# Kernel optimization log

Hardware: AMD Instinct MI355X
Metric: run time of the kernel (lower is better)

The kernel has to match this reference:

```python
import jax, jax.numpy as jnp
from jax import lax
import numpy as np

V, D, H, E, L, B = 512, 128, 64, 4, 60, 4096
ADJ = 184  # ((180 + 7) // 8) * 8


def setup_inputs() -> dict:
    key = jax.random.key(0)
    it = iter(jax.random.split(key, 64))

    def nrm(shape, s=0.05):
        return jax.random.normal(next(it), shape, dtype=jnp.float32) * s

    x = jax.random.randint(next(it), (B, L), 0, V, dtype=jnp.int32)
    inp = {"x": x, "emb": nrm((V, D), 0.02).at[0].set(0.0)}  # padding_idx=0 row zero
    for d in ("f", "r"):
        inp[f"w_ih_{d}"] = nrm((4 * H, D)); inp[f"w_hh_{d}"] = nrm((4 * H, H))
        inp[f"b_ih_{d}"] = nrm((4 * H,)); inp[f"b_hh_{d}"] = nrm((4 * H,))
    for p, i_, h_, o_ in (("e", 1, 16, 8), ("l", 1, 16, 8), ("c", V, 32, 16), ("p", 6, 24, 12), ("x", 4, 16, 8)):
        inp[f"{p}_w1"] = nrm((h_, i_)); inp[f"{p}_b1"] = nrm((h_,))
        inp[f"{p}_w2"] = nrm((o_, h_)); inp[f"{p}_b2"] = nrm((o_,))
    inp["fp_w"] = nrm((ADJ, 180)); inp["fp_b"] = nrm((ADJ,))
    inp["attn_w"] = nrm((3 * ADJ, ADJ)); inp["attn_b"] = nrm((3 * ADJ,))
    inp["out_w"] = nrm((ADJ, ADJ)); inp["out_b"] = nrm((ADJ,))
    for i, (o_, i_) in enumerate(((128, ADJ), (64, 128), (32, 64), (E, 32)), 1):
        inp[f"g_w{i}"] = nrm((o_, i_)); inp[f"g_b{i}"] = nrm((o_,))
    return inp


def _mlp2(h, w1, b1, w2, b2):
    return jnp.maximum(h @ w1.T + b1, 0.0) @ w2.T + b2


def _lstm_final(xe, w_ih, w_hh, b_ih, b_hh):
    # torch LSTM gate order i, f, g, o; returns final hidden state [B, H]
    xg = jnp.einsum('bld,gd->blg', xe, w_ih) + b_ih
    h0 = jnp.zeros((xe.shape[0], H), xe.dtype)

    def step(carry, g_t):
        h, c = carry
        g = g_t + h @ w_hh.T + b_hh
        i, f, gg, o = jnp.split(g, 4, axis=-1)
        c = jax.nn.sigmoid(f) * c + jax.nn.sigmoid(i) * jnp.tanh(gg)
        h = jax.nn.sigmoid(o) * jnp.tanh(c)
        return (h, c), None

    (h, _), _ = lax.scan(step, (h0, h0), jnp.swapaxes(xg, 0, 1))
    return h


def _sequence_stats(x):
    # Fully vectorized equivalent of the per-sequence python loops
    f32 = jnp.float32
    mask = x != 0
    vlen = mask.sum(1)                                       # [B]
    vlenf = jnp.maximum(vlen, 1).astype(f32)
    pos = jnp.arange(L)
    # per-row histogram over valid tokens (torch.bincount of valid_seq)
    counts = jnp.zeros((B, V), f32).at[jnp.arange(B)[:, None], x].add(mask.astype(f32))
    probs = counts / jnp.maximum(counts.sum(1, keepdims=True), 1.0)
    entropy = -jnp.sum(probs * jnp.log(probs + 1e-8), axis=1)
    entropy = jnp.where(vlen > 1, entropy, 0.0)
    char_dist = counts / vlenf[:, None]
    # compact valid tokens to the front (torch: seq[seq != 0]), stable argsort
    order = jnp.argsort((~mask).astype(jnp.int32), axis=1)
    cseq = jnp.take_along_axis(x, order, axis=1)
    cseq = jnp.where(pos[None] < vlen[:, None], cseq, 0)
    a, b = cseq[:, :-1], cseq[:, 1:]
    pairmask = pos[: L - 1][None] < (vlen - 1)[:, None]
    den1 = jnp.maximum(vlen - 1, 1).astype(f32)
    repeat = ((a == b) & pairmask).sum(1) / den1
    inc = ((b > a) & pairmask).sum(1) / den1
    dec = ((b < a) & pairmask).sum(1) / den1
    m2 = pos[: L - 2][None] < (vlen - 2)[:, None]
    per = ((cseq[:, :-2] == cseq[:, 2:]) & m2).sum(1) / jnp.maximum(vlen - 2, 1)
    per = jnp.where(vlen >= 4, per, 0.0)
    diversity = (counts > 0).sum(1) / vlenf
    # longest run of equal consecutive tokens via cummax of reset positions
    eq = jnp.concatenate([jnp.zeros((B, 1), bool), (cseq[:, 1:] == cseq[:, :-1]) & (pos[1:][None] < vlen[:, None])], 1)
    lastreset = lax.cummax(jnp.where(eq, -1, pos[None]), axis=1)
    runlen = pos[None] - lastreset + 1
    max_rep = jnp.where(pos[None] < vlen[:, None], runlen, 0).max(1) / vlenf
    pattern = jnp.stack([repeat, inc, dec, per, diversity, max_rep], 1).astype(f32)
    pattern = jnp.where((vlen > 1)[:, None], pattern, 0.0)
    # unique bigrams: sort pair codes, count distinct valid codes
    codes = jnp.where(pairmask, a * V + b, -1)
    s = jnp.sort(codes, axis=1)
    prevc = jnp.concatenate([jnp.full((B, 1), -2, s.dtype), s[:, :-1]], 1)
    comp_ratio = ((s != prevc) & (s >= 0)).sum(1) / den1
    info_density = entropy / jnp.log(jnp.maximum(vlen, 2).astype(f32))
    # local complexity: mean over sliding windows of (#unique / w), w = min(5, len//2)
    wsel = jnp.minimum(5, vlen // 2)
    local = jnp.zeros((B,), f32)
    for w in (2, 3, 4, 5):
        nwin = L - w + 1
        sh = [cseq[:, k:k + nwin] for k in range(w)]
        u = jnp.ones((B, nwin), f32)
        for k in range(1, w):
            isnew = jnp.ones((B, nwin), bool)
            for m in range(k):
                isnew = isnew & (sh[k] != sh[m])
            u = u + isnew
        winmask = pos[:nwin][None] < (vlen - w + 1)[:, None]
        lc = (u * winmask).sum(1) / w / jnp.maximum(vlen - w + 1, 1)
        local = jnp.where(wsel == w, lc, local)
    trans = 1.0 - repeat  # transitions/(len-1) == 1 - repeat_ratio
    complexity = jnp.stack([comp_ratio, info_density, local, trans], 1).astype(f32)
    complexity = jnp.where((vlen > 1)[:, None], complexity, 0.0)
    return entropy, vlen, char_dist, pattern, complexity


def reference(x, emb, w_ih_f, w_hh_f, b_ih_f, b_hh_f, w_ih_r, w_hh_r, b_ih_r, b_hh_r, e_w1, e_b1, e_w2, e_b2, l_w1, l_b1, l_w2, l_b2, c_w1, c_b1, c_w2, c_b2, p_w1, p_b1, p_w2, p_b2, x_w1, x_b1, x_w2, x_b2, fp_w, fp_b, attn_w, attn_b, out_w, out_b, g_w1, g_b1, g_w2, g_b2, g_w3, g_b3, g_w4, g_b4):
    entropy, vlen, char_dist, pattern, complexity = _sequence_stats(x)
    xe = emb[x]                                               # [B, L, D]
    h_f = _lstm_final(xe, w_ih_f, w_hh_f, b_ih_f, b_hh_f)
    h_r = _lstm_final(xe[:, ::-1], w_ih_r, w_hh_r, b_ih_r, b_hh_r)
    feats = jnp.concatenate([
        h_f, h_r,
        _mlp2((entropy / 4.0)[:, None], e_w1, e_b1, e_w2, e_b2),
        _mlp2((vlen.astype(jnp.float32) / 60.0)[:, None], l_w1, l_b1, l_w2, l_b2),
        _mlp2(char_dist, c_w1, c_b1, c_w2, c_b2),
        _mlp2(pattern, p_w1, p_b1, p_w2, p_b2),
        _mlp2(complexity, x_w1, x_b1, x_w2, x_b2),
    ], axis=1)                                                # [B, 180]
    f = feats @ fp_w.T + fp_b                                 # [B, 184]
    # MultiheadAttention with seq_len == 1: softmax over a single key is 1,
    # so attended = out_proj(v_proj(f)) exactly (q/k projections cancel).
    wv, bv = attn_w[2 * ADJ:], attn_b[2 * ADJ:]
    attended = (f @ wv.T + bv) @ out_w.T + out_b
    h = jnp.maximum(attended @ g_w1.T + g_b1, 0.0)
    h = jnp.maximum(h @ g_w2.T + g_b2, 0.0)
    h = jnp.maximum(h @ g_w3.T + g_b3, 0.0)
    logits = h @ g_w4.T + g_b4
    return jax.nn.softmax(logits, axis=-1)  # eval path (training=False)
```

## Files before the change

### kernel.cpp

```cpp
#include <hip/hip_runtime.h>

#define BATCH 4096
#define SEQL  60
#define VOC   512
#define EMBD  128
#define HID   64
#define GATES 256
#define ADJ   184

typedef __attribute__((ext_vector_type(8))) short short8;
typedef __attribute__((ext_vector_type(4))) float f32x4;

__device__ __forceinline__ float sigm(float x) {
  return __builtin_amdgcn_rcpf(1.f + __expf(-x));
}
__device__ __forceinline__ float tanh_(float x) {
  float e = __expf(2.f * x);
  return 1.f - 2.f * __builtin_amdgcn_rcpf(e + 1.f);
}
__device__ __forceinline__ unsigned short f2bf_rne(float f) {
  unsigned int u = __float_as_uint(f);
  unsigned int r = (u + 0x7fffu + ((u >> 16) & 1u)) >> 16;
  return (unsigned short)r;
}
__device__ __forceinline__ unsigned short f2bf(float f) {
  return (unsigned short)((__float_as_uint(f) + 0x8000u) >> 16);
}
__device__ __forceinline__ float dot4(float4 a, float4 b, float acc) {
  acc = fmaf(a.x, b.x, acc); acc = fmaf(a.y, b.y, acc);
  acc = fmaf(a.z, b.z, acc); acc = fmaf(a.w, b.w, acc);
  return acc;
}
__device__ __forceinline__ float wsumf(float v) {
  #pragma unroll
  for (int s = 32; s > 0; s >>= 1) v += __shfl_xor(v, s, 64);
  return v;
}
__device__ __forceinline__ int wsumi(int v) {
  #pragma unroll
  for (int s = 32; s > 0; s >>= 1) v += __shfl_xor(v, s, 64);
  return v;
}
__device__ __forceinline__ int wmaxi(int v) {
  #pragma unroll
  for (int s = 32; s > 0; s >>= 1) v = max(v, __shfl_xor(v, s, 64));
  return v;
}

__global__ __launch_bounds__(256) void k_prep(
    const float* __restrict__ emb,
    const float* __restrict__ wih_f, const float* __restrict__ bif, const float* __restrict__ bhf,
    const float* __restrict__ wih_r, const float* __restrict__ bir, const float* __restrict__ bhr,
    const float* __restrict__ whh_f, const float* __restrict__ whh_r,
    const float* __restrict__ g_w1, const float* __restrict__ g_b1,
    const float* __restrict__ out_w, const float* __restrict__ out_b,
    const float* __restrict__ attn_w, const float* __restrict__ attn_b,
    const float* __restrict__ fp_w, const float* __restrict__ fp_b,
    const float* __restrict__ g_w2, const float* __restrict__ g_w3,
    const float* __restrict__ g_w4, const float* __restrict__ c_w1,
    float* __restrict__ G_f, float* __restrict__ G_r,
    unsigned short* __restrict__ Wfrag,
    float* __restrict__ A, float* __restrict__ avb,
    float* __restrict__ Bp, float* __restrict__ vb,
    float* __restrict__ g_w2t, float* __restrict__ g_w3t, float* __restrict__ g_w4t,
    float* __restrict__ c_w1t) {
  const int bid = blockIdx.x;
  const int tid = threadIdx.x;

  if (bid < 128) {
    const int dir = bid >> 6;
    const int rem = bid & 63;
    const int v0 = (rem >> 2) * 32;
    const int j0 = (rem & 3) * 64;
    const float* W = dir ? wih_r : wih_f;
    const float* bi = dir ? bir : bif;
    const float* bh = dir ? bhr : bhf;
    float* G = dir ? G_r : G_f;
    const int vp = tid >> 4;
    const int jq = tid & 15;
    const int v = v0 + vp * 2;
    const int j = j0 + jq * 4;
    const int gg = j >> 6;
    const int u0 = j & 63;

    const float4* E0 = (const float4*)(emb + (size_t)v * 128);
    const float4* E1 = (const float4*)(emb + (size_t)(v + 1) * 128);
    const float4* W0 = (const float4*)(W + (size_t)j * 128);
    const float4* W1 = (const float4*)(W + (size_t)(j + 1) * 128);
    const float4* W2 = (const float4*)(W + (size_t)(j + 2) * 128);
    const float4* W3 = (const float4*)(W + (size_t)(j + 3) * 128);

    float a00 = 0.f, a01 = 0.f, a02 = 0.f, a03 = 0.f;
    float a10 = 0.f, a11 = 0.f, a12 = 0.f, a13 = 0.f;
    #pragma unroll 4
    for (int d4 = 0; d4 < 32; d4++) {
      float4 e0 = E0[d4], e1 = E1[d4];
      float4 w0 = W0[d4], w1 = W1[d4], w2 = W2[d4], w3 = W3[d4];
      a00 = dot4(e0, w0, a00); a01 = dot4(e0, w1, a01);
      a02 = dot4(e0, w2, a02); a03 = dot4(e0, w3, a03);
      a10 = dot4(e1, w0, a10); a11 = dot4(e1, w1, a11);
      a12 = dot4(e1, w2, a12); a13 = dot4(e1, w3, a13);
    }
    float b0v = bi[j] + bh[j], b1v = bi[j + 1] + bh[j + 1];
    float b2v = bi[j + 2] + bh[j + 2], b3v = bi[j + 3] + bh[j + 3];
    float* g0 = G + (size_t)v * 256 + u0 * 4 + gg;
    g0[0]  = a00 + b0v; g0[4]  = a01 + b1v;
    g0[8]  = a02 + b2v; g0[12] = a03 + b3v;
    float* g1 = g0 + 256;
    g1[0]  = a10 + b0v; g1[4]  = a11 + b1v;
    g1[8]  = a12 + b2v; g1[12] = a13 + b3v;
  } else if (bid < 144) {
    const int id = (bid - 128) * 256 + tid;
    const int lane = id & 63;
    const int fc = id >> 6;
    const int c = fc & 1;
    const int gg = (fc >> 1) & 3;
    const int w = (fc >> 3) & 3;
    const int dir = fc >> 5;
    const float* whh = dir ? whh_r : whh_f;
    const int n = gg * 64 + w * 16 + (lane & 15);
    const int kb = c * 32 + (lane >> 4) * 8;
    unsigned short* o = Wfrag + (size_t)id * 8;
    #pragma unroll
    for (int j = 0; j < 8; j++) o[j] = f2bf_rne(whh[n * 64 + kb + j]);
  } else if (bid < 272) {
    const int i = bid - 144;
    const int j = tid;
    const float* g1r = g_w1 + (size_t)i * ADJ;
    if (j < ADJ) {
      float a0 = 0.f, a1 = 0.f, a2 = 0.f, a3 = 0.f;
      for (int k = 0; k < ADJ; k += 4) {
        a0 = fmaf(g1r[k],     out_w[(size_t)(k)     * ADJ + j], a0);
        a1 = fmaf(g1r[k + 1], out_w[(size_t)(k + 1) * ADJ + j], a1);
        a2 = fmaf(g1r[k + 2], out_w[(size_t)(k + 2) * ADJ + j], a2);
        a3 = fmaf(g1r[k + 3], out_w[(size_t)(k + 3) * ADJ + j], a3);
      }
      A[(size_t)i * ADJ + j] = (a0 + a1) + (a2 + a3);
    } else if (j == ADJ) {
      float a0 = 0.f;
      for (int k = 0; k < ADJ; k++) a0 = fmaf(g1r[k], out_b[k], a0);
      avb[i] = a0 + g_b1[i];
    }
  } else if (bid < 456) {
    const int k = bid - 272;
    const int j = tid;
    const float* wvr = attn_w + (size_t)(2 * ADJ + k) * ADJ;
    if (j < 180) {
      float a0 = 0.f, a1 = 0.f, a2 = 0.f, a3 = 0.f;
      for (int m = 0; m < ADJ; m += 4) {
        a0 = fmaf(wvr[m],     fp_w[(size_t)(m)     * 180 + j], a0);
        a1 = fmaf(wvr[m + 1], fp_w[(size_t)(m + 1) * 180 + j], a1);
        a2 = fmaf(wvr[m + 2], fp_w[(size_t)(m + 2) * 180 + j], a2);
        a3 = fmaf(wvr[m + 3], fp_w[(size_t)(m + 3) * 180 + j], a3);
      }
      Bp[(size_t)k * 180 + j] = (a0 + a1) + (a2 + a3);
    } else if (j == 180) {
      float a0 = 0.f;
      for (int m = 0; m < ADJ; m++) a0 = fmaf(wvr[m], fp_b[m], a0);
      vb[k] = a0 + attn_b[2 * ADJ + k];
    }
  } else if (bid == 456) {
    for (int i = tid; i < 64 * 128; i += 256) {
      int o = i >> 7, k = i & 127;
      g_w2t[k * 64 + o] = g_w2[i];
    }
    for (int i = tid; i < 32 * 64; i += 256) {
      int o = i >> 6, k = i & 63;
      g_w3t[k * 32 + o] = g_w3[i];
    }
    if (tid < 128) {
      int o = tid >> 5, k = tid & 31;
      g_w4t[k * 4 + o] = g_w4[tid];
    }
  } else {
    const int base = (bid - 457) * 2048;
    for (int i = tid; i < 2048; i += 256) {
      int idx = base + i;
      int o = idx >> 9, k = idx & 511;
      c_w1t[k * 32 + o] = k ? c_w1[o * 512 + k] : 0.f;
    }
  }
}

#define LSTM_STEP(T, CUR, NXT)                                                 \
  {                                                                            \
    const unsigned short* hb = hbuf[(T) & 1];                                  \
    short8 a0 = *(const short8*)(hb + ln * 72 + kg * 8);                       \
    short8 a1 = *(const short8*)(hb + ln * 72 + 32 + kg * 8);                  \
    if ((T) < 59) {                                                            \
      int tsn = dir ? (58 - (T)) : ((T) + 1);                                  \
      uint4 of4 = *(const uint4*)(tokoff + tsn * 16 + kg * 4);                 \
      NXT[0] = *(const float4*)(Gb + of4.x + ub);                              \
      NXT[1] = *(const float4*)(Gb + of4.y + ub);                              \
      NXT[2] = *(const float4*)(Gb + of4.z + ub);                              \
      NXT[3] = *(const float4*)(Gb + of4.w + ub);                              \
    }                                                                          \
    f32x4 z0 = {0.f, 0.f, 0.f, 0.f};                                           \
    f32x4 acc0 = z0, acc1 = z0, acc2 = z0, acc3 = z0;                          \
    acc0 = __builtin_amdgcn_mfma_f32_16x16x32_bf16(a0, bfr[0][0], acc0, 0, 0, 0); \
    acc1 = __builtin_amdgcn_mfma_f32_16x16x32_bf16(a0, bfr[1][0], acc1, 0, 0, 0); \
    acc2 = __builtin_amdgcn_mfma_f32_16x16x32_bf16(a0, bfr[2][0], acc2, 0, 0, 0); \
    acc3 = __builtin_amdgcn_mfma_f32_16x16x32_bf16(a0, bfr[3][0], acc3, 0, 0, 0); \
    acc0 = __builtin_amdgcn_mfma_f32_16x16x32_bf16(a1, bfr[0][1], acc0, 0, 0, 0); \
    acc1 = __builtin_amdgcn_mfma_f32_16x16x32_bf16(a1, bfr[1][1], acc1, 0, 0, 0); \
    acc2 = __builtin_amdgcn_mfma_f32_16x16x32_bf16(a1, bfr[2][1], acc2, 0, 0, 0); \
    acc3 = __builtin_amdgcn_mfma_f32_16x16x32_bf16(a1, bfr[3][1], acc3, 0, 0, 0); \
    unsigned short* hw = hbuf[((T) + 1) & 1];                                  \
    _Pragma("unroll")                                                          \
    for (int r = 0; r < 4; r++) {                                              \
      float gi = acc0[r] + CUR[r].x;                                           \
      float gf = acc1[r] + CUR[r].y;                                           \
      float gc = acc2[r] + CUR[r].z;                                           \
      float go = acc3[r] + CUR[r].w;                                           \
      float cn = sigm(gf) * cst[r] + sigm(gi) * tanh_(gc);                     \
      cst[r] = cn;                                                             \
      float h = sigm(go) * tanh_(cn);                                          \
      hw[(kg * 4 + r) * 72 + u] = f2bf(h);                                     \
      if ((T) == 59) ho[(size_t)(b0 + kg * 4 + r) * 64 + u] = h;               \
    }                                                                          \
    __syncthreads();                                                           \
  }

__global__ __launch_bounds__(256) void k_main(
    const int* __restrict__ x,
    const float* __restrict__ G_f, const float* __restrict__ G_r,
    const unsigned short* __restrict__ Wfrag,
    const float* __restrict__ A, const float* __restrict__ avb,
    const float* __restrict__ Bp, const float* __restrict__ vb,
    float* __restrict__ C1t, float* __restrict__ c1b,
    float* __restrict__ hf_o, float* __restrict__ hr_o,
    float* __restrict__ ent_o, float* __restrict__ vlen_o,
    float* __restrict__ pat_o, float* __restrict__ cpx_o) {
  __shared__ __align__(16) unsigned short hbuf[2][16 * 72];
  __shared__ __align__(16) unsigned int tokoff[60 * 16];
  __shared__ unsigned int cnt[4][512];
  __shared__ unsigned short q[4][68];
  const int bid = blockIdx.x;
  const int tid = threadIdx.x;

  if (bid < 512) {
    const int lane = tid & 63;
    const int w = tid >> 6;
    const int dir = bid >> 8;
    const int blk = bid & 255;
    const int b0 = blk << 4;
    const float* G = dir ? G_r : G_f;
    const char* Gb = (const char*)G;
    float* ho = dir ? hr_o : hf_o;

    for (int i = tid; i < 960; i += 256) {
      int r = i / 60, t = i - r * 60;
      tokoff[t * 16 + r] = ((unsigned int)x[(size_t)(b0 + r) * 60 + t]) << 10;
    }
    for (int i = tid; i < 16 * 72; i += 256) hbuf[0][i] = 0;

    short8 bfr[4][2];
    #pragma unroll
    for (int gg = 0; gg < 4; gg++)
      #pragma unroll
      for (int c = 0; c < 2; c++) {
        int idx = (((dir * 4 + w) * 4 + gg) * 2 + c) * 64 + lane;
        bfr[gg][c] = *(const short8*)(Wfrag + (size_t)idx * 8);
      }

    const int kg = lane >> 4;
    const int ln = lane & 15;
    const int u = w * 16 + ln;
    const unsigned int ub = (unsigned int)u * 16;
    float cst[4] = {0.f, 0.f, 0.f, 0.f};
    float4 gvA[4], gvB[4];

    __syncthreads();

    {
      int ts0 = dir ? 59 : 0;
      uint4 of4 = *(const uint4*)(tokoff + ts0 * 16 + kg * 4);
      gvA[0] = *(const float4*)(Gb + of4.x + ub);
      gvA[1] = *(const float4*)(Gb + of4.y + ub);
      gvA[2] = *(const float4*)(Gb + of4.z + ub);
      gvA[3] = *(const float4*)(Gb + of4.w + ub);
    }

    #pragma unroll 1
    for (int tt = 0; tt < 30; tt++) {
      const int t0 = tt * 2, t1 = tt * 2 + 1;
      LSTM_STEP(t0, gvA, gvB)
      LSTM_STEP(t1, gvB, gvA)
    }
  } else if (bid < 1536) {
    const int lane = tid & 63;
    const int wid = tid >> 6;
    const int row = (bid - 512) * 4 + wid;
    unsigned int* cr = cnt[wid];
    unsigned short* qr = q[wid];

    for (int i = lane; i < 512; i += 64) cr[i] = 0u;
    qr[lane] = 0;
    if (lane < 4) qr[64 + lane] = 0;
    int v = (lane < 60) ? x[row * 60 + lane] : 0;
    bool act = (v != 0);
    unsigned long long amask = __ballot(act);
    int n = __popcll(amask);
    __syncthreads();
    if (act) {
      int pos = __popcll(amask & ((1ull << lane) - 1ull));
      qr[pos] = (unsigned short)v;
      atomicAdd(&cr[v], 1u);
    }
    __syncthreads();

    float vlenf = (float)(n >= 1 ? n : 1);
    float inv = 1.f / vlenf;

    float ent = 0.f; int distinct = 0;
    #pragma unroll
    for (int j = 0; j < 8; j++) {
      unsigned int c = cr[lane + j * 64];
      if (c) {
        distinct++;
        float p = (float)c * inv;
        ent -= p * __logf(p + 1e-8f);
      }
    }
    ent = wsumf(ent);
    distinct = wsumi(distinct);

    int a = qr[lane], b = qr[lane + 1], c2 = qr[lane + 2];
    bool v1 = (lane + 1 < n);
    bool v2 = (lane + 2 < n);
    int rep  = __popcll(__ballot(v1 && (a == b)));
    int incs = __popcll(__ballot(v1 && (b > a)));
    int decs = __popcll(__ballot(v1 && (b < a)));
    int per2 = __popcll(__ballot(v2 && (a == c2)));

    int prev = (lane > 0) ? (int)qr[lane - 1] : -1;
    bool isst = (lane < n) && (lane == 0 || a != prev);
    unsigned long long smask = __ballot(isst);
    int len = 0;
    if (isst) {
      unsigned long long hi = (lane < 63) ? (smask >> (lane + 1)) : 0ull;
      int next = hi ? (lane + __ffsll((unsigned long long)hi)) : n;
      len = next - lane;
    }
    int maxrun = wmaxi(len);

    int code = v1 ? (a * VOC + b) : -1;
    int unique = v1 ? 1 : 0;
    #pragma unroll 1
    for (int j = 0; j < 58; j++) {
      int cj = __shfl(code, j, 64);
      if (j < lane && cj == code) unique = 0;
    }
    int dc = __popcll(__ballot(unique != 0));

    int wl = n >> 1; if (wl > 5) wl = 5;
    float local = 0.f;
    if (wl >= 2) {
      bool pv = (lane + wl <= n);
      int u = 0;
      if (pv) {
        int t0 = qr[lane], t1 = qr[lane + 1], t2 = qr[lane + 2];
        int t3 = qr[lane + 3], t4 = qr[lane + 4];
        u = 1;
        u += (t1 != t0);
        if (wl >= 3) u += (int)((t2 != t1) && (t2 != t0));
        if (wl >= 4) u += (int)((t3 != t2) && (t3 != t1) && (t3 != t0));
        if (wl >= 5) u += (int)((t4 != t3) && (t4 != t2) && (t4 != t1) && (t4 != t0));
      }
      int usum = wsumi(u);
      int denw = n - wl + 1; if (denw < 1) denw = 1;
      local = (float)usum / (float)wl / (float)denw;
    }

    float den1 = (float)((n - 1) >= 1 ? (n - 1) : 1);
    float repeat = (float)rep / den1;
    float per = (n >= 4) ? (float)per2 / (float)((n - 2) >= 1 ? (n - 2) : 1) : 0.f;
    float entz = (n > 1) ? ent : 0.f;
    float z = (n > 1) ? 1.f : 0.f;

    if (lane == 0) {
      ent_o[row] = entz;
      vlen_o[row] = (float)n;
      pat_o[row * 6 + 0] = repeat * z;
      pat_o[row * 6 + 1] = (float)incs / den1 * z;
      pat_o[row * 6 + 2] = (float)decs / den1 * z;
      pat_o[row * 6 + 3] = per * z;
      pat_o[row * 6 + 4] = (float)distinct * inv * z;
      pat_o[row * 6 + 5] = (float)maxrun * inv * z;
      cpx_o[row * 4 + 0] = (float)dc / den1 * z;
      cpx_o[row * 4 + 1] = entz / __logf((float)(n >= 2 ? n : 2)) * z;
      cpx_o[row * 4 + 2] = local * z;
      cpx_o[row * 4 + 3] = (1.f - repeat) * z;
    }
  } else {
    const int i = bid - 1536, j = tid;
    const float* Ar = A + (size_t)i * ADJ;
    if (j < 180) {
      float a0 = 0.f, a1 = 0.f, a2 = 0.f, a3 = 0.f;
      for (int k = 0; k < ADJ; k += 4) {
        a0 = fmaf(Ar[k],     Bp[(size_t)(k)     * 180 + j], a0);
        a1 = fmaf(Ar[k + 1], Bp[(size_t)(k + 1) * 180 + j], a1);
        a2 = fmaf(Ar[k + 2], Bp[(size_t)(k + 2) * 180 + j], a2);
        a3 = fmaf(Ar[k + 3], Bp[(size_t)(k + 3) * 180 + j], a3);
      }
      C1t[(size_t)j * 128 + i] = (a0 + a1) + (a2 + a3);
    } else if (j == 180) {
      float a0 = 0.f;
      for (int k = 0; k < ADJ; k++) a0 = fmaf(Ar[k], vb[k], a0);
      c1b[i] = a0 + avb[i];
    }
  }
}

#define FSTR 192

__global__ __launch_bounds__(256) void k_head(
    const int* __restrict__ x,
    const float* __restrict__ hf, const float* __restrict__ hr,
    const float* __restrict__ ent, const float* __restrict__ vlen,
    const float* __restrict__ pat, const float* __restrict__ cpx,
    const float* __restrict__ e_w1, const float* __restrict__ e_b1,
    const float* __restrict__ e_w2, const float* __restrict__ e_b2,
    const float* __restrict__ l_w1, const float* __restrict__ l_b1,
    const float* __restrict__ l_w2, const float* __restrict__ l_b2,
    const float* __restrict__ c_w1t, const float* __restrict__ c_b1,
    const float* __restrict__ c_w2, const float* __restrict__ c_b2,
    const float* __restrict__ p_w1, const float* __restrict__ p_b1,
    const float* __restrict__ p_w2, const float* __restrict__ p_b2,
    const float* __restrict__ x_w1, const float* __restrict__ x_b1,
    const float* __restrict__ x_w2, const float* __restrict__ x_b2,
    const float* __restrict__ C1t, const float* __restrict__ c1b,
    const float* __restrict__ g_w2t, const float* __restrict__ g_b2,
    const float* __restrict__ g_w3t, const float* __restrict__ g_b3,
    const float* __restrict__ g_w4t, const float* __restrict__ g_b4,
    float* __restrict__ out) {
  __shared__ float feat[8 * FSTR];
  __shared__ unsigned short tk[8 * 64];
  __shared__ float h1[8 * 128];
  __shared__ float h2[8 * 64];
  __shared__ float h3[8 * 32];
  __shared__ float h1c[8 * 33];
  __shared__ float lg[32];
  const int tid = threadIdx.x;
  const int b0 = blockIdx.x * 8;

  if (tid < 128) {
    int r = tid >> 4, c = tid & 15;
    float4 vv = ((const float4*)(hf + (size_t)(b0 + r) * 64))[c];
    *(float4*)(feat + r * FSTR + c * 4) = vv;
  } else {
    int t = tid - 128;
    int r = t >> 4, c = t & 15;
    float4 vv = ((const float4*)(hr + (size_t)(b0 + r) * 64))[c];
    *(float4*)(feat + r * FSTR + 64 + c * 4) = vv;
  }
  for (int i = tid; i < 480; i += 256) {
    int r = i / 60, t = i - r * 60;
    tk[r * 64 + t] = (unsigned short)x[(size_t)(b0 + r) * 60 + t];
  }
  __syncthreads();
  {
    int o = tid & 31, r = tid >> 5;
    const unsigned short* tkr = tk + r * 64;
    float a0 = 0.f, a1 = 0.f, a2 = 0.f, a3 = 0.f;
    #pragma unroll 5
    for (int t = 0; t < 60; t += 4) {
      int t0 = tkr[t], t1 = tkr[t + 1], t2 = tkr[t + 2], t3 = tkr[t + 3];
      a0 += c_w1t[t0 * 32 + o];
      a1 += c_w1t[t1 * 32 + o];
      a2 += c_w1t[t2 * 32 + o];
      a3 += c_w1t[t3 * 32 + o];
    }
    float invv = __builtin_amdgcn_rcpf(fmaxf(vlen[b0 + r], 1.f));
    h1c[r * 33 + o] = fmaxf(((a0 + a1) + (a2 + a3)) * invv + c_b1[o], 0.f);
  }
  __syncthreads();
  if (tid < 32) {
    const int m = tid & 3, r = tid >> 2, b = b0 + r;
    float tt[24];
    if (m == 0) {
      float ein = ent[b] * 0.25f;
      #pragma unroll
      for (int o = 0; o < 16; o++) tt[o] = fmaxf(e_w1[o] * ein + e_b1[o], 0.f);
      #pragma unroll
      for (int o = 0; o < 8; o++) {
        float a = e_b2[o];
        #pragma unroll
        for (int k = 0; k < 16; k++) a = fmaf(e_w2[o * 16 + k], tt[k], a);
        feat[r * FSTR + 128 + o] = a;
      }
    } else if (m == 1) {
      float lin = vlen[b] * (1.f / 60.f);
      #pragma unroll
      for (int o = 0; o < 16; o++) tt[o] = fmaxf(l_w1[o] * lin + l_b1[o], 0.f);
      #pragma unroll
      for (int o = 0; o < 8; o++) {
        float a = l_b2[o];
        #pragma unroll
        for (int k = 0; k < 16; k++) a = fmaf(l_w2[o * 16 + k], tt[k], a);
        feat[r * FSTR + 136 + o] = a;
      }
    } else if (m == 2) {
      float pin[6];
      #pragma unroll
      for (int k = 0; k < 6; k++) pin[k] = pat[b * 6 + k];
      #pragma unroll
      for (int o = 0; o < 24; o++) {
        float a = p_b1[o];
        #pragma unroll
        for (int k = 0; k < 6; k++) a = fmaf(p_w1[o * 6 + k], pin[k], a);
        tt[o] = fmaxf(a, 0.f);
      }
      #pragma unroll
      for (int o = 0; o < 12; o++) {
        float a = p_b2[o];
        #pragma unroll
        for (int k = 0; k < 24; k++) a = fmaf(p_w2[o * 24 + k], tt[k], a);
        feat[r * FSTR + 160 + o] = a;
      }
    } else {
      float xin[4];
      #pragma unroll
      for (int k = 0; k < 4; k++) xin[k] = cpx[b * 4 + k];
      #pragma unroll
      for (int o = 0; o < 16; o++) {
        float a = x_b1[o];
        #pragma unroll
        for (int k = 0; k < 4; k++) a = fmaf(x_w1[o * 4 + k], xin[k], a);
        tt[o] = fmaxf(a, 0.f);
      }
      #pragma unroll
      for (int o = 0; o < 8; o++) {
        float a = x_b2[o];
        #pragma unroll
        for (int k = 0; k < 16; k++) a = fmaf(x_w2[o * 16 + k], tt[k], a);
        feat[r * FSTR + 172 + o] = a;
      }
    }
  } else if (tid >= 64 && tid < 192) {
    int t = tid - 64;
    int r = t >> 4, o = t & 15;
    float a = c_b2[o];
    const float* hh = h1c + r * 33;
    #pragma unroll
    for (int k = 0; k < 32; k++) a = fmaf(c_w2[o * 32 + k], hh[k], a);
    feat[r * FSTR + 144 + o] = a;
  }
  __syncthreads();

  {
    const int o = tid & 127, rg = tid >> 7;
    const float* f0p = feat + (rg * 4 + 0) * FSTR;
    const float* f1p = feat + (rg * 4 + 1) * FSTR;
    const float* f2p = feat + (rg * 4 + 2) * FSTR;
    const float* f3p = feat + (rg * 4 + 3) * FSTR;
    float a0 = 0.f, a1 = 0.f, a2 = 0.f, a3 = 0.f;
    #pragma unroll 3
    for (int k4 = 0; k4 < 45; k4++) {
      float w0 = C1t[(size_t)(k4 * 4 + 0) * 128 + o];
      float w1 = C1t[(size_t)(k4 * 4 + 1) * 128 + o];
      float w2 = C1t[(size_t)(k4 * 4 + 2) * 128 + o];
      float w3 = C1t[(size_t)(k4 * 4 + 3) * 128 + o];
      float4 f0 = *(const float4*)(f0p + k4 * 4);
      float4 f1 = *(const float4*)(f1p + k4 * 4);
      float4 f2 = *(const float4*)(f2p + k4 * 4);
      float4 f3 = *(const float4*)(f3p + k4 * 4);
      a0 = fmaf(w0, f0.x, a0); a0 = fmaf(w1, f0.y, a0);
      a0 = fmaf(w2, f0.z, a0); a0 = fmaf(w3, f0.w, a0);
      a1 = fmaf(w0, f1.x, a1); a1 = fmaf(w1, f1.y, a1);
      a1 = fmaf(w2, f1.z, a1); a1 = fmaf(w3, f1.w, a1);
      a2 = fmaf(w0, f2.x, a2); a2 = fmaf(w1, f2.y, a2);
      a2 = fmaf(w2, f2.z, a2); a2 = fmaf(w3, f2.w, a2);
      a3 = fmaf(w0, f3.x, a3); a3 = fmaf(w1, f3.y, a3);
      a3 = fmaf(w2, f3.z, a3); a3 = fmaf(w3, f3.w, a3);
    }
    float bb = c1b[o];
    h1[(rg * 4 + 0) * 128 + o] = fmaxf(a0 + bb, 0.f);
    h1[(rg * 4 + 1) * 128 + o] = fmaxf(a1 + bb, 0.f);
    h1[(rg * 4 + 2) * 128 + o] = fmaxf(a2 + bb, 0.f);
    h1[(rg * 4 + 3) * 128 + o] = fmaxf(a3 + bb, 0.f);
  }
  __syncthreads();
  {
    const int o = tid & 63, rg = tid >> 6;
    const float* f0p = h1 + (rg * 2 + 0) * 128;
    const float* f1p = h1 + (rg * 2 + 1) * 128;
    float a0 = 0.f, a1 = 0.f;
    #pragma unroll 4
    for (int k4 = 0; k4 < 32; k4++) {
      float w0 = g_w2t[(k4 * 4 + 0) * 64 + o];
      float w1 = g_w2t[(k4 * 4 + 1) * 64 + o];
      float w2 = g_w2t[(k4 * 4 + 2) * 64 + o];
      float w3 = g_w2t[(k4 * 4 + 3) * 64 + o];
      float4 f0 = *(const float4*)(f0p + k4 * 4);
      float4 f1 = *(const float4*)(f1p + k4 * 4);
      a0 = fmaf(w0, f0.x, a0); a0 = fmaf(w1, f0.y, a0);
      a0 = fmaf(w2, f0.z, a0); a0 = fmaf(w3, f0.w, a0);
      a1 = fmaf(w0, f1.x, a1); a1 = fmaf(w1, f1.y, a1);
      a1 = fmaf(w2, f1.z, a1); a1 = fmaf(w3, f1.w, a1);
    }
    float bb = g_b2[o];
    h2[(rg * 2 + 0) * 64 + o] = fmaxf(a0 + bb, 0.f);
    h2[(rg * 2 + 1) * 64 + o] = fmaxf(a1 + bb, 0.f);
  }
  __syncthreads();
  {
    const int o = tid & 31, rg = tid >> 5;
    const float* fp = h2 + rg * 64;
    float a = 0.f;
    #pragma unroll 4
    for (int k4 = 0; k4 < 16; k4++) {
      float w0 = g_w3t[(k4 * 4 + 0) * 32 + o];
      float w1 = g_w3t[(k4 * 4 + 1) * 32 + o];
      float w2 = g_w3t[(k4 * 4 + 2) * 32 + o];
      float w3 = g_w3t[(k4 * 4 + 3) * 32 + o];
      float4 f0 = *(const float4*)(fp + k4 * 4);
      a = fmaf(w0, f0.x, a); a = fmaf(w1, f0.y, a);
      a = fmaf(w2, f0.z, a); a = fmaf(w3, f0.w, a);
    }
    h3[rg * 32 + o] = fmaxf(a + g_b3[o], 0.f);
  }
  __syncthreads();
  if (tid < 32) {
    int r = tid >> 2, o = tid & 3;
    const float* hh = h3 + r * 32;
    float a = g_b4[o];
    #pragma unroll
    for (int k = 0; k < 32; k++) a = fmaf(g_w4t[k * 4 + o], hh[k], a);
    lg[tid] = a;
  }
  __syncthreads();
  if (tid < 8) {
    float l0 = lg[tid * 4 + 0], l1 = lg[tid * 4 + 1];
    float l2 = lg[tid * 4 + 2], l3 = lg[tid * 4 + 3];
    float m = fmaxf(fmaxf(l0, l1), fmaxf(l2, l3));
    float e0 = __expf(l0 - m), e1 = __expf(l1 - m);
    float e2 = __expf(l2 - m), e3 = __expf(l3 - m);
    float is = __builtin_amdgcn_rcpf(e0 + e1 + e2 + e3);
    float4 o4; o4.x = e0 * is; o4.y = e1 * is; o4.z = e2 * is; o4.w = e3 * is;
    *(float4*)(out + (size_t)(b0 + tid) * 4) = o4;
  }
}

extern "C" void kernel_launch(void* const* d_in, const int* in_sizes, int n_in,
                              void* d_out, int out_size, void* d_ws, size_t ws_size,
                              hipStream_t stream) {
  const int*   x     = (const int*)d_in[0];
  const float* emb   = (const float*)d_in[1];
  const float* wih_f = (const float*)d_in[2];
  const float* whh_f = (const float*)d_in[3];
  const float* bih_f = (const float*)d_in[4];
  const float* bhh_f = (const float*)d_in[5];
  const float* wih_r = (const float*)d_in[6];
  const float* whh_r = (const float*)d_in[7];
  const float* bih_r = (const float*)d_in[8];
  const float* bhh_r = (const float*)d_in[9];
  const float* e_w1 = (const float*)d_in[10]; const float* e_b1 = (const float*)d_in[11];
  const float* e_w2 = (const float*)d_in[12]; const float* e_b2 = (const float*)d_in[13];
  const float* l_w1 = (const float*)d_in[14]; const float* l_b1 = (const float*)d_in[15];
  const float* l_w2 = (const float*)d_in[16]; const float* l_b2 = (const float*)d_in[17];
  const float* c_w1 = (const float*)d_in[18]; const float* c_b1 = (const float*)d_in[19];
  const float* c_w2 = (const float*)d_in[20]; const float* c_b2 = (const float*)d_in[21];
  const float* p_w1 = (const float*)d_in[22]; const float* p_b1 = (const float*)d_in[23];
  const float* p_w2 = (const float*)d_in[24]; const float* p_b2 = (const float*)d_in[25];
  const float* x_w1 = (const float*)d_in[26]; const float* x_b1 = (const float*)d_in[27];
  const float* x_w2 = (const float*)d_in[28]; const float* x_b2 = (const float*)d_in[29];
  const float* fp_w = (const float*)d_in[30]; const float* fp_b = (const float*)d_in[31];
  const float* attn_w = (const float*)d_in[32]; const float* attn_b = (const float*)d_in[33];
  const float* out_w = (const float*)d_in[34]; const float* out_b = (const float*)d_in[35];
  const float* g_w1 = (const float*)d_in[36]; const float* g_b1 = (const float*)d_in[37];
  const float* g_w2 = (const float*)d_in[38]; const float* g_b2 = (const float*)d_in[39];
  const float* g_w3 = (const float*)d_in[40]; const float* g_b3 = (const float*)d_in[41];
  const float* g_w4 = (const float*)d_in[42]; const float* g_b4 = (const float*)d_in[43];

  float* ws   = (float*)d_ws;
  float* G_f  = ws;
  float* G_r  = G_f  + 512 * 256;
  float* hfw  = G_r  + 512 * 256;
  float* hrw  = hfw  + BATCH * 64;
  float* entw = hrw  + BATCH * 64;
  float* vlnw = entw + BATCH;
  float* patw = vlnw + BATCH;
  float* cpxw = patw + BATCH * 6;
  float* Aw   = cpxw + BATCH * 4;
  float* avbw = Aw + 128 * ADJ;
  float* Bpw  = avbw + 128;
  float* vbw  = Bpw + ADJ * 180;
  float* C1t  = vbw + ADJ;
  float* c1b  = C1t + 180 * 128;
  float* g2t  = c1b + 128;
  float* g3t  = g2t + 128 * 64;
  float* g4t  = g3t + 64 * 32;
  float* cw1t = g4t + 32 * 4;
  unsigned short* Wfrag = (unsigned short*)(cw1t + 512 * 32);

  k_prep<<<dim3(465), dim3(256), 0, stream>>>(
      emb, wih_f, bih_f, bhh_f, wih_r, bih_r, bhh_r, whh_f, whh_r,
      g_w1, g_b1, out_w, out_b, attn_w, attn_b, fp_w, fp_b,
      g_w2, g_w3, g_w4, c_w1,
      G_f, G_r, Wfrag, Aw, avbw, Bpw, vbw, g2t, g3t, g4t, cw1t);
  k_main<<<dim3(1664), dim3(256), 0, stream>>>(
      x, G_f, G_r, Wfrag, Aw, avbw, Bpw, vbw, C1t, c1b,
      hfw, hrw, entw, vlnw, patw, cpxw);
  k_head<<<dim3(BATCH / 8), dim3(256), 0, stream>>>(
      x, hfw, hrw, entw, vlnw, patw, cpxw,
      e_w1, e_b1, e_w2, e_b2, l_w1, l_b1, l_w2, l_b2,
      cw1t, c_b1, c_w2, c_b2, p_w1, p_b1, p_w2, p_b2,
      x_w1, x_b1, x_w2, x_b2, C1t, c1b,
      g2t, g_b2, g3t, g_b3, g4t, g_b4,
      (float*)d_out);
}
```

Before: 244.8 us.

## Prescale LSTM gates by log2e, swap MFMA operands, and vectorize hidden-state writes

Folds the log2(e) factors (doubled for the cell gate) into the precomputed input-gate table and the bf16 recurrent weight fragments, so the step uses raw exp2 and merges sigmoid*tanh pairs into a single reciprocal. The MFMA operands are swapped so each lane owns four consecutive hidden units of one batch row. This lets the gate-table reads come from one contiguous base, the bf16 hidden state go to LDS as one 8-byte store, and the final output go out as a float4. The goal is fewer transcendental and reciprocal ops and fewer memory instructions on the serial recurrence, at the cost of slightly different rounding and a clamp on the tanh exponent.

After: 248.0 us. About the same (+1.3%).

```diff
diff --git a/kernel.cpp b/kernel.cpp
--- a/kernel.cpp
+++ b/kernel.cpp
@@ -10,13 +10,17 @@
 
 typedef __attribute__((ext_vector_type(8))) short short8;
 typedef __attribute__((ext_vector_type(4))) float f32x4;
-
-__device__ __forceinline__ float sigm(float x) {
-  return __builtin_amdgcn_rcpf(1.f + __expf(-x));
-}
-__device__ __forceinline__ float tanh_(float x) {
-  float e = __expf(2.f * x);
-  return 1.f - 2.f * __builtin_amdgcn_rcpf(e + 1.f);
+typedef __attribute__((ext_vector_type(4))) unsigned short u16x4;
+
+#define L2E  1.4426950408889634f
+#define L2E2 2.8853900817779268f
+
+__device__ __forceinline__ float ex2(float x) {
+#if __has_builtin(__builtin_amdgcn_exp2f)
+  return __builtin_amdgcn_exp2f(x);
+#else
+  return exp2f(x);
+#endif
 }
 __device__ __forceinline__ unsigned short f2bf_rne(float f) {
   unsigned int u = __float_as_uint(f);
@@ -82,6 +86,7 @@
     const int j = j0 + jq * 4;
     const int gg = j >> 6;
     const int u0 = j & 63;
+    const float sc = (gg == 2) ? L2E2 : L2E;
 
     const float4* E0 = (const float4*)(emb + (size_t)v * 128);
     const float4* E1 = (const float4*)(emb + (size_t)(v + 1) * 128);
@@ -104,11 +109,11 @@
     float b0v = bi[j] + bh[j], b1v = bi[j + 1] + bh[j + 1];
     float b2v = bi[j + 2] + bh[j + 2], b3v = bi[j + 3] + bh[j + 3];
     float* g0 = G + (size_t)v * 256 + u0 * 4 + gg;
-    g0[0]  = a00 + b0v; g0[4]  = a01 + b1v;
-    g0[8]  = a02 + b2v; g0[12] = a03 + b3v;
+    g0[0]  = (a00 + b0v) * sc; g0[4]  = (a01 + b1v) * sc;
+    g0[8]  = (a02 + b2v) * sc; g0[12] = (a03 + b3v) * sc;
     float* g1 = g0 + 256;
-    g1[0]  = a10 + b0v; g1[4]  = a11 + b1v;
-    g1[8]  = a12 + b2v; g1[12] = a13 + b3v;
+    g1[0]  = (a10 + b0v) * sc; g1[4]  = (a11 + b1v) * sc;
+    g1[8]  = (a12 + b2v) * sc; g1[12] = (a13 + b3v) * sc;
   } else if (bid < 144) {
     const int id = (bid - 128) * 256 + tid;
     const int lane = id & 63;
@@ -118,11 +123,12 @@
     const int w = (fc >> 3) & 3;
     const int dir = fc >> 5;
     const float* whh = dir ? whh_r : whh_f;
+    const float sc = (gg == 2) ? L2E2 : L2E;
     const int n = gg * 64 + w * 16 + (lane & 15);
     const int kb = c * 32 + (lane >> 4) * 8;
     unsigned short* o = Wfrag + (size_t)id * 8;
     #pragma unroll
-    for (int j = 0; j < 8; j++) o[j] = f2bf_rne(whh[n * 64 + kb + j]);
+    for (int j = 0; j < 8; j++) o[j] = f2bf_rne(whh[n * 64 + kb + j] * sc);
   } else if (bid < 272) {
     const int i = bid - 144;
     const int j = tid;
@@ -185,38 +191,52 @@
 #define LSTM_STEP(T, CUR, NXT)                                                 \
   {                                                                            \
     const unsigned short* hb = hbuf[(T) & 1];                                  \
-    short8 a0 = *(const short8*)(hb + ln * 72 + kg * 8);                       \
-    short8 a1 = *(const short8*)(hb + ln * 72 + 32 + kg * 8);                  \
+    short8 hf0 = *(const short8*)(hb + rdoff);                                 \
+    short8 hf1 = *(const short8*)(hb + rdoff + 32);                            \
     if ((T) < 59) {                                                            \
       int tsn = dir ? (58 - (T)) : ((T) + 1);                                  \
-      uint4 of4 = *(const uint4*)(tokoff + tsn * 16 + kg * 4);                 \
-      NXT[0] = *(const float4*)(Gb + of4.x + ub);                              \
-      NXT[1] = *(const float4*)(Gb + of4.y + ub);                              \
-      NXT[2] = *(const float4*)(Gb + of4.z + ub);                              \
-      NXT[3] = *(const float4*)(Gb + of4.w + ub);                              \
+      const char* gp = Gb2 + tokoff[tsn * 16 + ln];                            \
+      NXT[0] = *(const float4*)(gp);                                           \
+      NXT[1] = *(const float4*)(gp + 16);                                      \
+      NXT[2] = *(const float4*)(gp + 32);                                      \
+      NXT[3] = *(const float4*)(gp + 48);                                      \
     }                                                                          \
     f32x4 z0 = {0.f, 0.f, 0.f, 0.f};                                           \
     f32x4 acc0 = z0, acc1 = z0, acc2 = z0, acc3 = z0;                          \
-    acc0 = __builtin_amdgcn_mfma_f32_16x16x32_bf16(a0, bfr[0][0], acc0, 0, 0, 0); \
-    acc1 = __builtin_amdgcn_mfma_f32_16x16x32_bf16(a0, bfr[1][0], acc1, 0, 0, 0); \
-    acc2 = __builtin_amdgcn_mfma_f32_16x16x32_bf16(a0, bfr[2][0], acc2, 0, 0, 0); \
-    acc3 = __builtin_amdgcn_mfma_f32_16x16x32_bf16(a0, bfr[3][0], acc3, 0, 0, 0); \
-    acc0 = __builtin_amdgcn_mfma_f32_16x16x32_bf16(a1, bfr[0][1], acc0, 0, 0, 0); \
-    acc1 = __builtin_amdgcn_mfma_f32_16x16x32_bf16(a1, bfr[1][1], acc1, 0, 0, 0); \
-    acc2 = __builtin_amdgcn_mfma_f32_16x16x32_bf16(a1, bfr[2][1], acc2, 0, 0, 0); \
-    acc3 = __builtin_amdgcn_mfma_f32_16x16x32_bf16(a1, bfr[3][1], acc3, 0, 0, 0); \
+    acc0 = __builtin_amdgcn_mfma_f32_16x16x32_bf16(bfr[0][0], hf0, acc0, 0, 0, 0); \
+    acc1 = __builtin_amdgcn_mfma_f32_16x16x32_bf16(bfr[1][0], hf0, acc1, 0, 0, 0); \
+    acc2 = __builtin_amdgcn_mfma_f32_16x16x32_bf16(bfr[2][0], hf0, acc2, 0, 0, 0); \
+    acc3 = __builtin_amdgcn_mfma_f32_16x16x32_bf16(bfr[3][0], hf0, acc3, 0, 0, 0); \
+    acc0 = __builtin_amdgcn_mfma_f32_16x16x32_bf16(bfr[0][1], hf1, acc0, 0, 0, 0); \
+    acc1 = __builtin_amdgcn_mfma_f32_16x16x32_bf16(bfr[1][1], hf1, acc1, 0, 0, 0); \
+    acc2 = __builtin_amdgcn_mfma_f32_16x16x32_bf16(bfr[2][1], hf1, acc2, 0, 0, 0); \
+    acc3 = __builtin_amdgcn_mfma_f32_16x16x32_bf16(bfr[3][1], hf1, acc3, 0, 0, 0); \
     unsigned short* hw = hbuf[((T) + 1) & 1];                                  \
+    unsigned short hh[4];                                                      \
     _Pragma("unroll")                                                          \
     for (int r = 0; r < 4; r++) {                                              \
       float gi = acc0[r] + CUR[r].x;                                           \
       float gf = acc1[r] + CUR[r].y;                                           \
       float gc = acc2[r] + CUR[r].z;                                           \
       float go = acc3[r] + CUR[r].w;                                           \
-      float cn = sigm(gf) * cst[r] + sigm(gi) * tanh_(gc);                     \
+      float Ef = ex2(-gf);                                                     \
+      float E1 = ex2(-gi);                                                     \
+      float E2 = ex2(gc);                                                      \
+      float sf = __builtin_amdgcn_rcpf(1.f + Ef);                              \
+      float p  = (E2 - 1.f) * __builtin_amdgcn_rcpf((1.f + E1) * (E2 + 1.f));  \
+      float cn = fmaf(sf, cst[r], p);                                          \
       cst[r] = cn;                                                             \
-      float h = sigm(go) * tanh_(cn);                                          \
-      hw[(kg * 4 + r) * 72 + u] = f2bf(h);                                     \
-      if ((T) == 59) ho[(size_t)(b0 + kg * 4 + r) * 64 + u] = h;               \
+      float E3 = ex2(-go);                                                     \
+      float E4 = ex2(fminf(L2E2 * cn, 126.f));                                 \
+      float h  = (E4 - 1.f) * __builtin_amdgcn_rcpf((1.f + E3) * (E4 + 1.f));  \
+      hv[r] = h;                                                               \
+      hh[r] = f2bf(h);                                                         \
+    }                                                                          \
+    u16x4 hvv = {hh[0], hh[1], hh[2], hh[3]};                                  \
+    *(u16x4*)(hw + wroff) = hvv;                                               \
+    if ((T) == 59) {                                                           \
+      float4 o4; o4.x = hv[0]; o4.y = hv[1]; o4.z = hv[2]; o4.w = hv[3];       \
+      *(float4*)(hop) = o4;                                                    \
     }                                                                          \
     __syncthreads();                                                           \
   }
@@ -245,7 +265,6 @@
     const int blk = bid & 255;
     const int b0 = blk << 4;
     const float* G = dir ? G_r : G_f;
-    const char* Gb = (const char*)G;
     float* ho = dir ? hr_o : hf_o;
 
     for (int i = tid; i < 960; i += 256) {
@@ -265,20 +284,24 @@
 
     const int kg = lane >> 4;
     const int ln = lane & 15;
-    const int u = w * 16 + ln;
-    const unsigned int ub = (unsigned int)u * 16;
+    const int ub2 = w * 16 + kg * 4;
+    const int rdoff = ln * 72 + kg * 8;
+    const int wroff = ln * 72 + ub2;
+    const char* Gb2 = (const char*)G + (size_t)ub2 * 16;
+    float* hop = ho + (size_t)(b0 + ln) * 64 + ub2;
     float cst[4] = {0.f, 0.f, 0.f, 0.f};
     float4 gvA[4], gvB[4];
+    float hv[4];
 
     __syncthreads();
 
     {
       int ts0 = dir ? 59 : 0;
-      uint4 of4 = *(const uint4*)(tokoff + ts0 * 16 + kg * 4);
-      gvA[0] = *(const float4*)(Gb + of4.x + ub);
-      gvA[1] = *(const float4*)(Gb + of4.y + ub);
-      gvA[2] = *(const float4*)(Gb + of4.z + ub);
-      gvA[3] = *(const float4*)(Gb + of4.w + ub);
+      const char* gp = Gb2 + tokoff[ts0 * 16 + ln];
+      gvA[0] = *(const float4*)(gp);
+      gvA[1] = *(const float4*)(gp + 16);
+      gvA[2] = *(const float4*)(gp + 32);
+      gvA[3] = *(const float4*)(gp + 48);
     }
 
     #pragma unroll 1
```
